# Kernel tuning notes

Measured on AMD Instinct MI355X. Metric: run time of the kernel, lower is better.

Reference implementation:

```python
import jax, jax.numpy as jnp
import numpy as np

T, H, I, E, K = 2048, 1024, 768, 16, 4

def setup_inputs() -> dict:
    key = jax.random.key(0)
    k1, k2, k3, k4, k5 = jax.random.split(key, 5)
    hidden_states = jax.random.normal(k1, (T, H), dtype=jnp.float32)
    top_k_index = jax.random.randint(k2, (T, K), 0, E, dtype=jnp.int64)
    top_k_weights = jax.random.uniform(k3, (T, K), dtype=jnp.float32)
    gate_up_proj = jax.random.normal(k4, (E, 2 * I, H), dtype=jnp.float32) * 0.02
    down_proj = jax.random.normal(k5, (E, H, I), dtype=jnp.float32) * 0.02
    return {"hidden_states": hidden_states, "top_k_index": top_k_index,
            "top_k_weights": top_k_weights, "gate_up_proj": gate_up_proj,
            "down_proj": down_proj}

def reference(hidden_states, top_k_index, top_k_weights, gate_up_proj, down_proj):
    # Masked dense MoE: scan over experts, each expert does full-token GEMMs
    # and a per-token combine weight (sum of routing weights where routed to e).
    # index_add over token_idx == sum over k of (mask * weight) * expert_out.
    n_experts = gate_up_proj.shape[0]

    def body(acc, xs):
        w_gu, w_d, e = xs  # [2I,H], [H,I], scalar
        gu = hidden_states @ w_gu.T                 # [T, 2I]
        gate, up = jnp.split(gu, 2, axis=-1)        # [T, I] each
        h = jax.nn.silu(gate) * up                  # [T, I]
        out = h @ w_d.T                             # [T, H]
        w_tok = jnp.sum(jnp.where(top_k_index == e, top_k_weights, 0.0), axis=-1)  # [T]
        return acc + out * w_tok[:, None], None

    acc0 = jnp.zeros_like(hidden_states)
    final, _ = jax.lax.scan(body, acc0, (gate_up_proj, down_proj, jnp.arange(n_experts)))
    return final
```

## Files before the change

kernel.cpp:

```cpp
#include <hip/hip_runtime.h>
#include <hip/hip_bf16.h>
#include <stdint.h>

#define T_TOK 2048
#define H_DIM 1024
#define I_DIM 768
#define E_NUM 16
#define K_TOP 4
#define NSLOT (T_TOK * K_TOP)
#define PSLOT 10240
#define NTILE 80

typedef short  s16x8 __attribute__((ext_vector_type(8)));
typedef float  f32x4 __attribute__((ext_vector_type(4)));
typedef unsigned short u16x8 __attribute__((ext_vector_type(8)));

#define MEMFENCE asm volatile("" ::: "memory")

__device__ __forceinline__ void gload16(const void* g, void* l) {
  __builtin_amdgcn_global_load_lds(
      (const __attribute__((address_space(1))) uint32_t*)g,
      (__attribute__((address_space(3))) uint32_t*)l, 16, 0, 0);
}

__device__ __forceinline__ unsigned short f2bf(float f) {
  __hip_bfloat16 h = __float2bfloat16(f);
  return *reinterpret_cast<unsigned short*>(&h);
}

__device__ __forceinline__ void write_b_row(char* bregion, int r, int half,
                                            f32x4 f0, f32x4 f1, f32x4 f2, f32x4 f3) {
  u16x8 c0, c1;
  c0[0]=f2bf(f0[0]); c0[1]=f2bf(f0[1]); c0[2]=f2bf(f0[2]); c0[3]=f2bf(f0[3]);
  c0[4]=f2bf(f1[0]); c0[5]=f2bf(f1[1]); c0[6]=f2bf(f1[2]); c0[7]=f2bf(f1[3]);
  c1[0]=f2bf(f2[0]); c1[1]=f2bf(f2[1]); c1[2]=f2bf(f2[2]); c1[3]=f2bf(f2[3]);
  c1[4]=f2bf(f3[0]); c1[5]=f2bf(f3[1]); c1[6]=f2bf(f3[2]); c1[7]=f2bf(f3[3]);
  int xr = (r >> 1) & 3;
  char* wb = bregion + r * 64;
  *(u16x8*)(wb + (((2*half + 0) ^ xr) * 16)) = c0;
  *(u16x8*)(wb + (((2*half + 1) ^ xr) * 16)) = c1;
}

__global__ __launch_bounds__(256) void cvt_bf16_kernel(
    const float* __restrict__ in, unsigned short* __restrict__ out, int n8) {
  int i = blockIdx.x * 256 + threadIdx.x;
  if (i >= n8) return;
  const float4* p = (const float4*)in;
  float4 a = p[2 * (size_t)i];
  float4 b = p[2 * (size_t)i + 1];
  u16x8 o;
  o[0] = f2bf(a.x); o[1] = f2bf(a.y); o[2] = f2bf(a.z); o[3] = f2bf(a.w);
  o[4] = f2bf(b.x); o[5] = f2bf(b.y); o[6] = f2bf(b.z); o[7] = f2bf(b.w);
  *(u16x8*)(out + (size_t)i * 8) = o;
}

__global__ __launch_bounds__(256) void route_kernel(
    const int* __restrict__ idx, const float* __restrict__ wts,
    int* __restrict__ slot_tok, float* __restrict__ slot_w,
    int* __restrict__ slot_of, int* __restrict__ tile_expert) {
  __shared__ int cnt[256][16];
  __shared__ int tot[16];
  __shared__ int pb[17];
  int tid = threadIdx.x;

  for (int e = 0; e < 16; ++e) cnt[tid][e] = 0;
  const int s0 = tid * 32;
  for (int i = 0; i < 32; ++i) {
    int e = idx[s0 + i] & 15;
    cnt[tid][e]++;
  }
  __syncthreads();
  if (tid < 16) {
    int run = 0;
    for (int c = 0; c < 256; ++c) { int v = cnt[c][tid]; cnt[c][tid] = run; run += v; }
    tot[tid] = run;
  }
  __syncthreads();
  if (tid == 0) {
    int acc = 0;
    for (int e = 0; e < 16; ++e) { pb[e] = acc; acc += (tot[e] + 127) & ~127; }
    pb[16] = acc;
  }
  __syncthreads();
  for (int p = tid; p < PSLOT; p += 256) { slot_tok[p] = 0; slot_w[p] = 0.0f; }
  if (tid < NTILE) {
    int ef = -1;
    for (int e = 0; e < 16; ++e)
      if (tid * 128 >= pb[e] && tid * 128 < pb[e + 1]) ef = e;
    tile_expert[tid] = ef;
  }
  __syncthreads();
  for (int i = 0; i < 32; ++i) {
    int s = s0 + i;
    int e = idx[s] & 15;
    int pos = pb[e] + cnt[tid][e]++;
    slot_tok[pos] = s >> 2;
    slot_w[pos]   = wts[s];
    slot_of[s]    = pos;
  }
}


__global__ __launch_bounds__(256) void gemm1_kernel(
    const unsigned short* __restrict__ Xbf,
    const float* __restrict__ Wgu,
    const int* __restrict__ slot_tok,
    const int* __restrict__ tile_expert,
    unsigned short* __restrict__ hbuf) {
  int bid  = blockIdx.y * 12 + blockIdx.x;
  int sbid = (bid & 7) * 120 + (bid >> 3);
  int by   = sbid / 12;
  int bx   = sbid % 12;
  int e = tile_expert[by];
  if (e < 0) return;
  int m0 = by * 128;
  int tid = threadIdx.x;
  int lane = tid & 63, w = tid >> 6;
  int wr = w >> 1, wc = w & 1;

  __shared__ short lds[2 * 8192];
  char* buf0 = (char*)lds;
  char* buf1 = buf0 + 16384;

  int srow = tid >> 2;
  int swzc = ((tid & 3) ^ ((tid >> 3) & 3)) * 16;
  int tok0 = slot_tok[m0 + srow];
  int tok1 = slot_tok[m0 + 64 + srow];
  const char* gA0 = (const char*)(Xbf + (size_t)tok0 * H_DIM) + swzc;
  const char* gA1 = (const char*)(Xbf + (size_t)tok1 * H_DIM) + swzc;

  int brow = tid >> 1;
  int half = tid & 1;
  int prow = (brow < 64) ? (bx * 64 + brow) : (768 + bx * 64 + (brow - 64));
  const float* gB = Wgu + ((size_t)e * 1536 + prow) * H_DIM + half * 16;

  int pswz = ((lane >> 4) ^ (((lane & 15) >> 1) & 3)) * 8;

  f32x4 accg[4][2] = {};
  f32x4 accu[4][2] = {};
  f32x4 s0_0, s0_1, s0_2, s0_3, s1_0, s1_1, s1_2, s1_3;
  f32x4 s2_0, s2_1, s2_2, s2_3, s3_0, s3_1, s3_2, s3_3;

#define NT1 32
#define A_GLOAD1(kt, bufp) do {                               \
    int kk_ = (kt) < NT1 ? (kt) : NT1 - 1;                    \
    int ko_ = kk_ * 64;                                       \
    gload16(gA0 + ko_, (bufp) + tid * 16);                    \
    gload16(gA1 + ko_, (bufp) + 4096 + tid * 16);             \
  } while (0)
#define B_LOAD1(v0, v1, v2, v3, kt) do {                      \
    int kk_ = (kt) < NT1 ? (kt) : NT1 - 1;                    \
    const f32x4* p_ = (const f32x4*)(gB + (size_t)kk_ * 32);  \
    v0 = p_[0]; v1 = p_[1]; v2 = p_[2]; v3 = p_[3];           \
  } while (0)

#define G1_COMPUTE(bufp) do {                                                          \
    const short* La = (const short*)(bufp);                                            \
    s16x8 af[4], bgf[2], buf2[2];                                                      \
    _Pragma("unroll")                                                                  \
    for (int mi = 0; mi < 4; ++mi)                                                     \
      af[mi] = *(const s16x8*)(La + (wr * 64 + mi * 16 + (lane & 15)) * 32 + pswz);    \
    _Pragma("unroll")                                                                  \
    for (int ni = 0; ni < 2; ++ni) {                                                   \
      int row = wc * 32 + ni * 16 + (lane & 15);                                       \
      bgf[ni]  = *(const s16x8*)(La + 4096 + row * 32 + pswz);                         \
      buf2[ni] = *(const s16x8*)(La + 6144 + row * 32 + pswz);                         \
    }                                                                                  \
    _Pragma("unroll")                                                                  \
    for (int mi = 0; mi < 4; ++mi)                                                     \
      _Pragma("unroll")                                                                \
      for (int ni = 0; ni < 2; ++ni) {                                                 \
        accg[mi][ni] = __builtin_amdgcn_mfma_f32_16x16x32_bf16(af[mi], bgf[ni],  accg[mi][ni], 0, 0, 0); \
        accu[mi][ni] = __builtin_amdgcn_mfma_f32_16x16x32_bf16(af[mi], buf2[ni], accu[mi][ni], 0, 0, 0); \
      }                                                                                \
  } while (0)

#define ITER1(kt, wv0, wv1, wv2, wv3, lv0, lv1, lv2, lv3) do {  \
    char* cbuf_ = ((kt) & 1) ? buf1 : buf0;                     \
    char* nbuf_ = ((kt) & 1) ? buf0 : buf1;                     \
    MEMFENCE;                                                   \
    A_GLOAD1((kt) + 1, nbuf_);                                  \
    MEMFENCE;                                                   \
    B_LOAD1(lv0, lv1, lv2, lv3, (kt) + 3);                      \
    asm volatile("s_waitcnt vmcnt(10)" ::: "memory");           \
    write_b_row(nbuf_ + 8192, brow, half, wv0, wv1, wv2, wv3);  \
    asm volatile("s_waitcnt lgkmcnt(0)" ::: "memory");          \
    __builtin_amdgcn_s_barrier();                               \
    MEMFENCE;                                                   \
    G1_COMPUTE(cbuf_);                                          \
    MEMFENCE;                                                   \
    __builtin_amdgcn_s_barrier();                               \
  } while (0)

  A_GLOAD1(0, buf0);
  MEMFENCE;
  B_LOAD1(s0_0, s0_1, s0_2, s0_3, 0);
  MEMFENCE;
  B_LOAD1(s1_0, s1_1, s1_2, s1_3, 1);
  MEMFENCE;
  B_LOAD1(s2_0, s2_1, s2_2, s2_3, 2);
  asm volatile("s_waitcnt vmcnt(8)" ::: "memory");
  write_b_row(buf0 + 8192, brow, half, s0_0, s0_1, s0_2, s0_3);

  for (int kt = 0; kt < NT1; kt += 4) {
    ITER1(kt + 0, s1_0, s1_1, s1_2, s1_3, s3_0, s3_1, s3_2, s3_3);
    ITER1(kt + 1, s2_0, s2_1, s2_2, s2_3, s0_0, s0_1, s0_2, s0_3);
    ITER1(kt + 2, s3_0, s3_1, s3_2, s3_3, s1_0, s1_1, s1_2, s1_3);
    ITER1(kt + 3, s0_0, s0_1, s0_2, s0_3, s2_0, s2_1, s2_2, s2_3);
  }
#undef ITER1
#undef G1_COMPUTE
#undef B_LOAD1
#undef A_GLOAD1

#pragma unroll
  for (int mi = 0; mi < 4; ++mi) {
#pragma unroll
    for (int ni = 0; ni < 2; ++ni) {
      int col = bx * 64 + wc * 32 + ni * 16 + (lane & 15);
#pragma unroll
      for (int q = 0; q < 4; ++q) {
        int m = m0 + wr * 64 + mi * 16 + (lane >> 4) * 4 + q;
        float g = accg[mi][ni][q];
        float u = accu[mi][ni][q];
        float s = g / (1.0f + __expf(-g));
        hbuf[(size_t)m * I_DIM + col] = f2bf(s * u);
      }
    }
  }
}

__global__ __launch_bounds__(256) void gemm2_kernel(
    const unsigned short* __restrict__ hbuf,
    const float* __restrict__ Wd,
    const int* __restrict__ slot_tok,
    const float* __restrict__ slot_w,
    const int* __restrict__ tile_expert,
    float* __restrict__ y) {
  int bid  = blockIdx.y * 8 + blockIdx.x;
  int sbid = (bid & 7) * 80 + (bid >> 3);
  int by   = sbid >> 3;
  int bx   = sbid & 7;
  int e = tile_expert[by];
  if (e < 0) return;
  int m0 = by * 128;
  int tid = threadIdx.x;
  int lane = tid & 63, w = tid >> 6;
  int wr = w >> 1, wc = w & 1;

  __shared__ short lds[2 * 8192];
  char* buf0 = (char*)lds;
  char* buf1 = buf0 + 16384;

  int srow = tid >> 2;
  int swzc = ((tid & 3) ^ ((tid >> 3) & 3)) * 16;
  const char* gA0 = (const char*)(hbuf + (size_t)(m0 + srow) * I_DIM) + swzc;
  const char* gA1 = (const char*)(hbuf + (size_t)(m0 + 64 + srow) * I_DIM) + swzc;

  int brow = tid >> 1;
  int half = tid & 1;
  const float* gB = Wd + ((size_t)e * 1024 + bx * 128 + brow) * I_DIM + half * 16;

  int pswz = ((lane >> 4) ^ (((lane & 15) >> 1) & 3)) * 8;

  f32x4 acc[4][4] = {};
  f32x4 s0_0, s0_1, s0_2, s0_3, s1_0, s1_1, s1_2, s1_3;
  f32x4 s2_0, s2_1, s2_2, s2_3, s3_0, s3_1, s3_2, s3_3;

#define NT2 24
#define A_GLOAD2(kt, bufp) do {                               \
    int kk_ = (kt) < NT2 ? (kt) : NT2 - 1;                    \
    int ko_ = kk_ * 64;                                       \
    gload16(gA0 + ko_, (bufp) + tid * 16);                    \
    gload16(gA1 + ko_, (bufp) + 4096 + tid * 16);             \
  } while (0)
#define B_LOAD2(v0, v1, v2, v3, kt) do {                      \
    int kk_ = (kt) < NT2 ? (kt) : NT2 - 1;                    \
    const f32x4* p_ = (const f32x4*)(gB + (size_t)kk_ * 32);  \
    v0 = p_[0]; v1 = p_[1]; v2 = p_[2]; v3 = p_[3];           \
  } while (0)

#define G2_COMPUTE(bufp) do {                                                          \
    const short* La = (const short*)(bufp);                                            \
    s16x8 af[4], bf[4];                                                                \
    _Pragma("unroll")                                                                  \
    for (int mi = 0; mi < 4; ++mi)                                                     \
      af[mi] = *(const s16x8*)(La + (wr * 64 + mi * 16 + (lane & 15)) * 32 + pswz);    \
    _Pragma("unroll")                                                                  \
    for (int ni = 0; ni < 4; ++ni)                                                     \
      bf[ni] = *(const s16x8*)(La + 4096 + (wc * 64 + ni * 16 + (lane & 15)) * 32 + pswz); \
    _Pragma("unroll")                                                                  \
    for (int mi = 0; mi < 4; ++mi)                                                     \
      _Pragma("unroll")                                                                \
      for (int ni = 0; ni < 4; ++ni)                                                   \
        acc[mi][ni] = __builtin_amdgcn_mfma_f32_16x16x32_bf16(af[mi], bf[ni], acc[mi][ni], 0, 0, 0); \
  } while (0)

#define ITER2(kt, wv0, wv1, wv2, wv3, lv0, lv1, lv2, lv3) do {  \
    char* cbuf_ = ((kt) & 1) ? buf1 : buf0;                     \
    char* nbuf_ = ((kt) & 1) ? buf0 : buf1;                     \
    MEMFENCE;                                                   \
    A_GLOAD2((kt) + 1, nbuf_);                                  \
    MEMFENCE;                                                   \
    B_LOAD2(lv0, lv1, lv2, lv3, (kt) + 3);                      \
    asm volatile("s_waitcnt vmcnt(10)" ::: "memory");           \
    write_b_row(nbuf_ + 8192, brow, half, wv0, wv1, wv2, wv3);  \
    asm volatile("s_waitcnt lgkmcnt(0)" ::: "memory");          \
    __builtin_amdgcn_s_barrier();                               \
    MEMFENCE;                                                   \
    G2_COMPUTE(cbuf_);                                          \
    MEMFENCE;                                                   \
    __builtin_amdgcn_s_barrier();                               \
  } while (0)

  A_GLOAD2(0, buf0);
  MEMFENCE;
  B_LOAD2(s0_0, s0_1, s0_2, s0_3, 0);
  MEMFENCE;
  B_LOAD2(s1_0, s1_1, s1_2, s1_3, 1);
  MEMFENCE;
  B_LOAD2(s2_0, s2_1, s2_2, s2_3, 2);
  asm volatile("s_waitcnt vmcnt(8)" ::: "memory");
  write_b_row(buf0 + 8192, brow, half, s0_0, s0_1, s0_2, s0_3);

  for (int kt = 0; kt < NT2; kt += 4) {
    ITER2(kt + 0, s1_0, s1_1, s1_2, s1_3, s3_0, s3_1, s3_2, s3_3);
    ITER2(kt + 1, s2_0, s2_1, s2_2, s2_3, s0_0, s0_1, s0_2, s0_3);
    ITER2(kt + 2, s3_0, s3_1, s3_2, s3_3, s1_0, s1_1, s1_2, s1_3);
    ITER2(kt + 3, s0_0, s0_1, s0_2, s0_3, s2_0, s2_1, s2_2, s2_3);
  }
#undef ITER2
#undef G2_COMPUTE
#undef B_LOAD2
#undef A_GLOAD2

#pragma unroll
  for (int mi = 0; mi < 4; ++mi) {
#pragma unroll
    for (int q = 0; q < 4; ++q) {
      int m = m0 + wr * 64 + mi * 16 + (lane >> 4) * 4 + q;
      float wgt = slot_w[m];
      float* orow = y + (size_t)m * H_DIM + bx * 128 + wc * 64 + (lane & 15);
#pragma unroll
      for (int ni = 0; ni < 4; ++ni)
        orow[ni * 16] = acc[mi][ni][q] * wgt;
    }
  }
}

__global__ __launch_bounds__(256) void combine_kernel(
    const float* __restrict__ y, const int* __restrict__ slot_of,
    float* __restrict__ out) {
  int t = blockIdx.x;
  int c = threadIdx.x * 4;
  int s0 = slot_of[t * 4 + 0], s1 = slot_of[t * 4 + 1];
  int s2 = slot_of[t * 4 + 2], s3 = slot_of[t * 4 + 3];
  f32x4 v0 = *(const f32x4*)(y + (size_t)s0 * H_DIM + c);
  f32x4 v1 = *(const f32x4*)(y + (size_t)s1 * H_DIM + c);
  f32x4 v2 = *(const f32x4*)(y + (size_t)s2 * H_DIM + c);
  f32x4 v3 = *(const f32x4*)(y + (size_t)s3 * H_DIM + c);
  f32x4 r = (v0 + v1) + (v2 + v3);
  *(f32x4*)(out + (size_t)t * H_DIM + c) = r;
}

extern "C" void kernel_launch(void* const* d_in, const int* in_sizes, int n_in,
                              void* d_out, int out_size, void* d_ws, size_t ws_size,
                              hipStream_t stream) {
  const float* hs       = (const float*)d_in[0];
  const int*   topk_idx = (const int*)d_in[1];
  const float* topk_w   = (const float*)d_in[2];
  const float* w_gu     = (const float*)d_in[3];
  const float* w_d      = (const float*)d_in[4];
  float* out = (float*)d_out;

  char* ws = (char*)d_ws;
  unsigned short* Xbf  = (unsigned short*)(ws);
  unsigned short* hbuf = (unsigned short*)(ws + 4194304);
  float*          y    = (float*)(ws + 19922944);
  int*   slot_tok    = (int*)(ws + 61865984);
  float* slot_w      = (float*)(ws + 61906944);
  int*   slot_of     = (int*)(ws + 61947904);
  int*   tile_expert = (int*)(ws + 61980672);

  cvt_bf16_kernel<<<1024, 256, 0, stream>>>(hs, Xbf, T_TOK * H_DIM / 8);
  route_kernel<<<1, 256, 0, stream>>>(topk_idx, topk_w, slot_tok, slot_w, slot_of, tile_expert);

  gemm1_kernel<<<dim3(12, NTILE), 256, 0, stream>>>(Xbf, w_gu, slot_tok, tile_expert, hbuf);
  gemm2_kernel<<<dim3(8, NTILE), 256, 0, stream>>>(hbuf, w_d, slot_tok, slot_w, tile_expert, y);
  combine_kernel<<<T_TOK, 256, 0, stream>>>(y, slot_of, out);
}
```

Before: 135.4 us.

## Pre-convert gate/up weights to K-tiled bf16 and enlarge gemm1 tiles

Adds a per-call kernel that converts the fp32 gate/up weights to bf16 in a K-major tiled layout, so gemm1 can stream both operands straight into LDS with direct global-to-LDS loads. gemm1 moves to 256x256 tiles with 512 threads, a 64-wide K step and double buffering in 128 KB of LDS. Routing now pads experts to 256 rows and emits a separate 128-row tile map for gemm2. The extra conversion pass reads and writes about 100 MB of weights every call, which competes with the gains from cheaper loads and fewer redundant B fetches.

After: 155.8 us. 1.15x slower.

```diff
diff --git a/kernel.cpp b/kernel.cpp
--- a/kernel.cpp
+++ b/kernel.cpp
@@ -7,13 +7,16 @@
 #define I_DIM 768
 #define E_NUM 16
 #define K_TOP 4
-#define NSLOT (T_TOK * K_TOP)
-#define PSLOT 10240
-#define NTILE 80
+#define NSLOT 8192
+#define PSLOT 12288
+#define NT256 48
+#define NT128 96
+#define RTOT_GU 24576
 
 typedef short  s16x8 __attribute__((ext_vector_type(8)));
 typedef float  f32x4 __attribute__((ext_vector_type(4)));
 typedef unsigned short u16x8 __attribute__((ext_vector_type(8)));
+typedef unsigned short u16x4 __attribute__((ext_vector_type(4)));
 
 #define MEMFENCE asm volatile("" ::: "memory")
 
@@ -26,19 +29,6 @@
 __device__ __forceinline__ unsigned short f2bf(float f) {
   __hip_bfloat16 h = __float2bfloat16(f);
   return *reinterpret_cast<unsigned short*>(&h);
-}
-
-__device__ __forceinline__ void write_b_row(char* bregion, int r, int half,
-                                            f32x4 f0, f32x4 f1, f32x4 f2, f32x4 f3) {
-  u16x8 c0, c1;
-  c0[0]=f2bf(f0[0]); c0[1]=f2bf(f0[1]); c0[2]=f2bf(f0[2]); c0[3]=f2bf(f0[3]);
-  c0[4]=f2bf(f1[0]); c0[5]=f2bf(f1[1]); c0[6]=f2bf(f1[2]); c0[7]=f2bf(f1[3]);
-  c1[0]=f2bf(f2[0]); c1[1]=f2bf(f2[1]); c1[2]=f2bf(f2[2]); c1[3]=f2bf(f2[3]);
-  c1[4]=f2bf(f3[0]); c1[5]=f2bf(f3[1]); c1[6]=f2bf(f3[2]); c1[7]=f2bf(f3[3]);
-  int xr = (r >> 1) & 3;
-  char* wb = bregion + r * 64;
-  *(u16x8*)(wb + (((2*half + 0) ^ xr) * 16)) = c0;
-  *(u16x8*)(wb + (((2*half + 1) ^ xr) * 16)) = c1;
 }
 
 __global__ __launch_bounds__(256) void cvt_bf16_kernel(
@@ -54,10 +44,34 @@
   *(u16x8*)(out + (size_t)i * 8) = o;
 }
 
+__global__ __launch_bounds__(256) void wtrans_kernel(
+    const float* __restrict__ in, unsigned short* __restrict__ out,
+    int K, int RTOT) {
+  __shared__ unsigned short tile[16 * 1024];
+  int r0 = blockIdx.x * 16;
+  int t = threadIdx.x;
+  int nf4 = 16 * K / 4;
+  const f32x4* src = (const f32x4*)(in + (size_t)r0 * K);
+  for (int i = t; i < nf4; i += 256) {
+    f32x4 v = src[i];
+    u16x4 o;
+    o[0] = f2bf(v[0]); o[1] = f2bf(v[1]); o[2] = f2bf(v[2]); o[3] = f2bf(v[3]);
+    *(u16x4*)(tile + (size_t)i * 4) = o;
+  }
+  __syncthreads();
+  int nkt = K / 64;
+  int row = t >> 4, k4 = (t & 15) * 4;
+  for (int kt = 0; kt < nkt; ++kt) {
+    u16x4 v = *(const u16x4*)(tile + row * K + kt * 64 + k4);
+    *(u16x4*)(out + ((size_t)kt * RTOT + r0 + row) * 64 + k4) = v;
+  }
+}
+
 __global__ __launch_bounds__(256) void route_kernel(
     const int* __restrict__ idx, const float* __restrict__ wts,
     int* __restrict__ slot_tok, float* __restrict__ slot_w,
-    int* __restrict__ slot_of, int* __restrict__ tile_expert) {
+    int* __restrict__ slot_of, int* __restrict__ tile_expert,
+    int* __restrict__ tile_expert128) {
   __shared__ int cnt[256][16];
   __shared__ int tot[16];
   __shared__ int pb[17];
@@ -78,16 +92,23 @@
   __syncthreads();
   if (tid == 0) {
     int acc = 0;
-    for (int e = 0; e < 16; ++e) { pb[e] = acc; acc += (tot[e] + 127) & ~127; }
+    for (int e = 0; e < 16; ++e) { pb[e] = acc; acc += (tot[e] + 255) & ~255; }
     pb[16] = acc;
   }
   __syncthreads();
   for (int p = tid; p < PSLOT; p += 256) { slot_tok[p] = 0; slot_w[p] = 0.0f; }
-  if (tid < NTILE) {
+  if (tid < NT256) {
     int ef = -1;
     for (int e = 0; e < 16; ++e)
-      if (tid * 128 >= pb[e] && tid * 128 < pb[e + 1]) ef = e;
+      if (tid * 256 >= pb[e] && tid * 256 < pb[e + 1]) ef = e;
     tile_expert[tid] = ef;
+  }
+  if (tid >= 64 && tid < 64 + NT128) {
+    int m = (tid - 64) * 128;
+    int ef = -1;
+    for (int e = 0; e < 16; ++e)
+      if (m >= pb[e] && m < pb[e + 1]) ef = e;
+    tile_expert128[tid - 64] = ef;
   }
   __syncthreads();
   for (int i = 0; i < 32; ++i) {
@@ -100,127 +121,111 @@
   }
 }
 
-
-__global__ __launch_bounds__(256) void gemm1_kernel(
+__global__ __launch_bounds__(512) void gemm1_kernel(
     const unsigned short* __restrict__ Xbf,
-    const float* __restrict__ Wgu,
+    const unsigned short* __restrict__ WguK,
     const int* __restrict__ slot_tok,
     const int* __restrict__ tile_expert,
     unsigned short* __restrict__ hbuf) {
-  int bid  = blockIdx.y * 12 + blockIdx.x;
-  int sbid = (bid & 7) * 120 + (bid >> 3);
-  int by   = sbid / 12;
-  int bx   = sbid % 12;
+  __shared__ char lds[131072];
+
+  int bid  = blockIdx.y * 6 + blockIdx.x;
+  int sbid = (bid & 7) * 36 + (bid >> 3);
+  int by = sbid / 6, bx = sbid % 6;
   int e = tile_expert[by];
   if (e < 0) return;
-  int m0 = by * 128;
-  int tid = threadIdx.x;
-  int lane = tid & 63, w = tid >> 6;
-  int wr = w >> 1, wc = w & 1;
-
-  __shared__ short lds[2 * 8192];
-  char* buf0 = (char*)lds;
-  char* buf1 = buf0 + 16384;
-
-  int srow = tid >> 2;
-  int swzc = ((tid & 3) ^ ((tid >> 3) & 3)) * 16;
-  int tok0 = slot_tok[m0 + srow];
-  int tok1 = slot_tok[m0 + 64 + srow];
-  const char* gA0 = (const char*)(Xbf + (size_t)tok0 * H_DIM) + swzc;
-  const char* gA1 = (const char*)(Xbf + (size_t)tok1 * H_DIM) + swzc;
-
-  int brow = tid >> 1;
-  int half = tid & 1;
-  int prow = (brow < 64) ? (bx * 64 + brow) : (768 + bx * 64 + (brow - 64));
-  const float* gB = Wgu + ((size_t)e * 1536 + prow) * H_DIM + half * 16;
-
-  int pswz = ((lane >> 4) ^ (((lane & 15) >> 1) & 3)) * 8;
-
-  f32x4 accg[4][2] = {};
-  f32x4 accu[4][2] = {};
-  f32x4 s0_0, s0_1, s0_2, s0_3, s1_0, s1_1, s1_2, s1_3;
-  f32x4 s2_0, s2_1, s2_2, s2_3, s3_0, s3_1, s3_2, s3_3;
-
-#define NT1 32
-#define A_GLOAD1(kt, bufp) do {                               \
-    int kk_ = (kt) < NT1 ? (kt) : NT1 - 1;                    \
-    int ko_ = kk_ * 64;                                       \
-    gload16(gA0 + ko_, (bufp) + tid * 16);                    \
-    gload16(gA1 + ko_, (bufp) + 4096 + tid * 16);             \
-  } while (0)
-#define B_LOAD1(v0, v1, v2, v3, kt) do {                      \
-    int kk_ = (kt) < NT1 ? (kt) : NT1 - 1;                    \
-    const f32x4* p_ = (const f32x4*)(gB + (size_t)kk_ * 32);  \
-    v0 = p_[0]; v1 = p_[1]; v2 = p_[2]; v3 = p_[3];           \
-  } while (0)
-
-#define G1_COMPUTE(bufp) do {                                                          \
-    const short* La = (const short*)(bufp);                                            \
-    s16x8 af[4], bgf[2], buf2[2];                                                      \
-    _Pragma("unroll")                                                                  \
-    for (int mi = 0; mi < 4; ++mi)                                                     \
-      af[mi] = *(const s16x8*)(La + (wr * 64 + mi * 16 + (lane & 15)) * 32 + pswz);    \
-    _Pragma("unroll")                                                                  \
-    for (int ni = 0; ni < 2; ++ni) {                                                   \
-      int row = wc * 32 + ni * 16 + (lane & 15);                                       \
-      bgf[ni]  = *(const s16x8*)(La + 4096 + row * 32 + pswz);                         \
-      buf2[ni] = *(const s16x8*)(La + 6144 + row * 32 + pswz);                         \
-    }                                                                                  \
-    _Pragma("unroll")                                                                  \
-    for (int mi = 0; mi < 4; ++mi)                                                     \
-      _Pragma("unroll")                                                                \
-      for (int ni = 0; ni < 2; ++ni) {                                                 \
-        accg[mi][ni] = __builtin_amdgcn_mfma_f32_16x16x32_bf16(af[mi], bgf[ni],  accg[mi][ni], 0, 0, 0); \
-        accu[mi][ni] = __builtin_amdgcn_mfma_f32_16x16x32_bf16(af[mi], buf2[ni], accu[mi][ni], 0, 0, 0); \
-      }                                                                                \
-  } while (0)
-
-#define ITER1(kt, wv0, wv1, wv2, wv3, lv0, lv1, lv2, lv3) do {  \
-    char* cbuf_ = ((kt) & 1) ? buf1 : buf0;                     \
-    char* nbuf_ = ((kt) & 1) ? buf0 : buf1;                     \
-    MEMFENCE;                                                   \
-    A_GLOAD1((kt) + 1, nbuf_);                                  \
-    MEMFENCE;                                                   \
-    B_LOAD1(lv0, lv1, lv2, lv3, (kt) + 3);                      \
-    asm volatile("s_waitcnt vmcnt(10)" ::: "memory");           \
-    write_b_row(nbuf_ + 8192, brow, half, wv0, wv1, wv2, wv3);  \
-    asm volatile("s_waitcnt lgkmcnt(0)" ::: "memory");          \
-    __builtin_amdgcn_s_barrier();                               \
-    MEMFENCE;                                                   \
-    G1_COMPUTE(cbuf_);                                          \
-    MEMFENCE;                                                   \
-    __builtin_amdgcn_s_barrier();                               \
-  } while (0)
-
-  A_GLOAD1(0, buf0);
+  int m0 = by * 256;
+  int t = threadIdx.x;
+  int lane = t & 63, w = t >> 6;
+  int wr = w >> 2, wc = w & 3;
+  int l15 = lane & 15, lhi = lane >> 4;
+
+  int rr = t >> 3;
+  int lslot16 = ((t & 7) ^ (rr & 7)) * 16;
+  const char* aS[4];
+#pragma unroll
+  for (int a = 0; a < 4; ++a) {
+    int tok = slot_tok[m0 + a * 64 + rr];
+    aS[a] = (const char*)Xbf + (size_t)tok * 2048 + lslot16;
+  }
+  const char* bS[4];
+#pragma unroll
+  for (int c = 0; c < 4; ++c) {
+    int rg = e * 1536 + ((c < 2) ? 0 : 768) + bx * 128 + (c & 1) * 64 + rr;
+    bS[c] = (const char*)WguK + (size_t)rg * 128 + lslot16;
+  }
+
+  f32x4 accg[8][2] = {};
+  f32x4 accu[8][2] = {};
+
+#define G1_STAGE(bi, kt) do {                                 \
+    char* dst = lds + (bi) * 65536 + t * 16;                  \
+    size_t ao = (size_t)(kt) * 128;                           \
+    size_t bo = (size_t)(kt) * ((size_t)RTOT_GU * 128);       \
+    MEMFENCE;                                                 \
+    gload16(aS[0] + ao, dst);                                 \
+    gload16(aS[1] + ao, dst + 8192);                          \
+    gload16(aS[2] + ao, dst + 16384);                         \
+    gload16(aS[3] + ao, dst + 24576);                         \
+    gload16(bS[0] + bo, dst + 32768);                         \
+    gload16(bS[1] + bo, dst + 40960);                         \
+    gload16(bS[2] + bo, dst + 49152);                         \
+    gload16(bS[3] + bo, dst + 57344);                         \
+    MEMFENCE;                                                 \
+  } while (0)
+
+#define G1_COMPUTE(bi) do {                                                        \
+    const short* La = (const short*)(lds + (bi) * 65536);                          \
+    const short* Lb = La + 16384;                                                  \
+    _Pragma("unroll")                                                              \
+    for (int ks = 0; ks < 2; ++ks) {                                               \
+      int p8 = (((ks) * 4 + lhi) ^ (l15 & 7)) * 8;                                 \
+      s16x8 af[8], bg[2], bu[2];                                                   \
+      _Pragma("unroll")                                                            \
+      for (int mi = 0; mi < 8; ++mi)                                               \
+        af[mi] = *(const s16x8*)(La + (wr * 128 + mi * 16 + l15) * 64 + p8);       \
+      _Pragma("unroll")                                                            \
+      for (int ni = 0; ni < 2; ++ni) {                                             \
+        bg[ni] = *(const s16x8*)(Lb + (wc * 32 + ni * 16 + l15) * 64 + p8);        \
+        bu[ni] = *(const s16x8*)(Lb + (128 + wc * 32 + ni * 16 + l15) * 64 + p8);  \
+      }                                                                            \
+      __builtin_amdgcn_s_setprio(1);                                               \
+      _Pragma("unroll")                                                            \
+      for (int mi = 0; mi < 8; ++mi)                                               \
+        _Pragma("unroll")                                                          \
+        for (int ni = 0; ni < 2; ++ni) {                                           \
+          accg[mi][ni] = __builtin_amdgcn_mfma_f32_16x16x32_bf16(af[mi], bg[ni], accg[mi][ni], 0, 0, 0); \
+          accu[mi][ni] = __builtin_amdgcn_mfma_f32_16x16x32_bf16(af[mi], bu[ni], accu[mi][ni], 0, 0, 0); \
+        }                                                                          \
+      __builtin_amdgcn_s_setprio(0);                                               \
+    }                                                                              \
+  } while (0)
+
+  G1_STAGE(0, 0);
+  asm volatile("s_waitcnt vmcnt(0)" ::: "memory");
+  __builtin_amdgcn_s_barrier();
   MEMFENCE;
-  B_LOAD1(s0_0, s0_1, s0_2, s0_3, 0);
-  MEMFENCE;
-  B_LOAD1(s1_0, s1_1, s1_2, s1_3, 1);
-  MEMFENCE;
-  B_LOAD1(s2_0, s2_1, s2_2, s2_3, 2);
-  asm volatile("s_waitcnt vmcnt(8)" ::: "memory");
-  write_b_row(buf0 + 8192, brow, half, s0_0, s0_1, s0_2, s0_3);
-
-  for (int kt = 0; kt < NT1; kt += 4) {
-    ITER1(kt + 0, s1_0, s1_1, s1_2, s1_3, s3_0, s3_1, s3_2, s3_3);
-    ITER1(kt + 1, s2_0, s2_1, s2_2, s2_3, s0_0, s0_1, s0_2, s0_3);
-    ITER1(kt + 2, s3_0, s3_1, s3_2, s3_3, s1_0, s1_1, s1_2, s1_3);
-    ITER1(kt + 3, s0_0, s0_1, s0_2, s0_3, s2_0, s2_1, s2_2, s2_3);
-  }
-#undef ITER1
+
+  int cur = 0;
+  for (int kt = 0; kt < 16; ++kt) {
+    if (kt + 1 < 16) G1_STAGE(cur ^ 1, kt + 1);
+    G1_COMPUTE(cur);
+    asm volatile("s_waitcnt vmcnt(0)" ::: "memory");
+    __builtin_amdgcn_s_barrier();
+    MEMFENCE;
+    cur ^= 1;
+  }
+#undef G1_STAGE
 #undef G1_COMPUTE
-#undef B_LOAD1
-#undef A_GLOAD1
-
-#pragma unroll
-  for (int mi = 0; mi < 4; ++mi) {
+
+#pragma unroll
+  for (int mi = 0; mi < 8; ++mi) {
 #pragma unroll
     for (int ni = 0; ni < 2; ++ni) {
-      int col = bx * 64 + wc * 32 + ni * 16 + (lane & 15);
+      int col = bx * 128 + wc * 32 + ni * 16 + l15;
 #pragma unroll
       for (int q = 0; q < 4; ++q) {
-        int m = m0 + wr * 64 + mi * 16 + (lane >> 4) * 4 + q;
+        int m = m0 + wr * 128 + mi * 16 + lhi * 4 + q;
         float g = accg[mi][ni][q];
         float u = accu[mi][ni][q];
         float s = g / (1.0f + __expf(-g));
@@ -235,13 +240,13 @@
     const float* __restrict__ Wd,
     const int* __restrict__ slot_tok,
     const float* __restrict__ slot_w,
-    const int* __restrict__ tile_expert,
+    const int* __restrict__ tile_expert128,
     float* __restrict__ y) {
   int bid  = blockIdx.y * 8 + blockIdx.x;
-  int sbid = (bid & 7) * 80 + (bid >> 3);
+  int sbid = (bid & 7) * 96 + (bid >> 3);
   int by   = sbid >> 3;
   int bx   = sbid & 7;
-  int e = tile_expert[by];
+  int e = tile_expert128[by];
   if (e < 0) return;
   int m0 = by * 128;
   int tid = threadIdx.x;
@@ -266,6 +271,18 @@
   f32x4 acc[4][4] = {};
   f32x4 s0_0, s0_1, s0_2, s0_3, s1_0, s1_1, s1_2, s1_3;
   f32x4 s2_0, s2_1, s2_2, s2_3, s3_0, s3_1, s3_2, s3_3;
+
+#define WR_BROW(bregion, r, h_, f0, f1, f2, f3) do {          \
+    u16x8 c0, c1;                                             \
+    c0[0]=f2bf(f0[0]); c0[1]=f2bf(f0[1]); c0[2]=f2bf(f0[2]); c0[3]=f2bf(f0[3]); \
+    c0[4]=f2bf(f1[0]); c0[5]=f2bf(f1[1]); c0[6]=f2bf(f1[2]); c0[7]=f2bf(f1[3]); \
+    c1[0]=f2bf(f2[0]); c1[1]=f2bf(f2[1]); c1[2]=f2bf(f2[2]); c1[3]=f2bf(f2[3]); \
+    c1[4]=f2bf(f3[0]); c1[5]=f2bf(f3[1]); c1[6]=f2bf(f3[2]); c1[7]=f2bf(f3[3]); \
+    int xr = ((r) >> 1) & 3;                                  \
+    char* wb = (bregion) + (r) * 64;                          \
+    *(u16x8*)(wb + (((2*(h_) + 0) ^ xr) * 16)) = c0;          \
+    *(u16x8*)(wb + (((2*(h_) + 1) ^ xr) * 16)) = c1;          \
+  } while (0)
 
 #define NT2 24
 #define A_GLOAD2(kt, bufp) do {                               \
@@ -304,7 +321,7 @@
     MEMFENCE;                                                   \
     B_LOAD2(lv0, lv1, lv2, lv3, (kt) + 3);                      \
     asm volatile("s_waitcnt vmcnt(10)" ::: "memory");           \
-    write_b_row(nbuf_ + 8192, brow, half, wv0, wv1, wv2, wv3);  \
+    WR_BROW(nbuf_ + 8192, brow, half, wv0, wv1, wv2, wv3);      \
     asm volatile("s_waitcnt lgkmcnt(0)" ::: "memory");          \
     __builtin_amdgcn_s_barrier();                               \
     MEMFENCE;                                                   \
@@ -321,7 +338,7 @@
   MEMFENCE;
   B_LOAD2(s2_0, s2_1, s2_2, s2_3, 2);
   asm volatile("s_waitcnt vmcnt(8)" ::: "memory");
-  write_b_row(buf0 + 8192, brow, half, s0_0, s0_1, s0_2, s0_3);
+  WR_BROW(buf0 + 8192, brow, half, s0_0, s0_1, s0_2, s0_3);
 
   for (int kt = 0; kt < NT2; kt += 4) {
     ITER2(kt + 0, s1_0, s1_1, s1_2, s1_3, s3_0, s3_1, s3_2, s3_3);
@@ -333,6 +350,7 @@
 #undef G2_COMPUTE
 #undef B_LOAD2
 #undef A_GLOAD2
+#undef WR_BROW
 
 #pragma unroll
   for (int mi = 0; mi < 4; ++mi) {
@@ -375,17 +393,21 @@
 
   char* ws = (char*)d_ws;
   unsigned short* Xbf  = (unsigned short*)(ws);
-  unsigned short* hbuf = (unsigned short*)(ws + 4194304);
-  float*          y    = (float*)(ws + 19922944);
-  int*   slot_tok    = (int*)(ws + 61865984);
-  float* slot_w      = (float*)(ws + 61906944);
-  int*   slot_of     = (int*)(ws + 61947904);
-  int*   tile_expert = (int*)(ws + 61980672);
+  unsigned short* WguK = (unsigned short*)(ws + 4194304);
+  float*          y    = (float*)(ws + 4194304);
+  unsigned short* hbuf = (unsigned short*)(ws + 54525952);
+  int*   slot_tok       = (int*)(ws + 73400320);
+  float* slot_w         = (float*)(ws + 73449472);
+  int*   slot_of        = (int*)(ws + 73498624);
+  int*   tile_expert    = (int*)(ws + 73531392);
+  int*   tile_expert128 = (int*)(ws + 73531648);
 
   cvt_bf16_kernel<<<1024, 256, 0, stream>>>(hs, Xbf, T_TOK * H_DIM / 8);
-  route_kernel<<<1, 256, 0, stream>>>(topk_idx, topk_w, slot_tok, slot_w, slot_of, tile_expert);
-
-  gemm1_kernel<<<dim3(12, NTILE), 256, 0, stream>>>(Xbf, w_gu, slot_tok, tile_expert, hbuf);
-  gemm2_kernel<<<dim3(8, NTILE), 256, 0, stream>>>(hbuf, w_d, slot_tok, slot_w, tile_expert, y);
+  route_kernel<<<1, 256, 0, stream>>>(topk_idx, topk_w, slot_tok, slot_w,
+                                      slot_of, tile_expert, tile_expert128);
+  wtrans_kernel<<<RTOT_GU / 16, 256, 0, stream>>>(w_gu, WguK, H_DIM, RTOT_GU);
+
+  gemm1_kernel<<<dim3(6, NT256), 512, 0, stream>>>(Xbf, WguK, slot_tok, tile_expert, hbuf);
+  gemm2_kernel<<<dim3(8, NT128), 256, 0, stream>>>(hbuf, w_d, slot_tok, slot_w, tile_expert128, y);
   combine_kernel<<<T_TOK, 256, 0, stream>>>(y, slot_of, out);
 }
```

## Enlarge grouped-GEMM M tile to 256 rows with 256-padded expert segments

Applied to the files above, without the earlier changes.

Routing now pads each expert's slot range to multiples of 256, and both grouped GEMMs use 256-row tiles (8 M-fragments per wave) instead of 128. Each streamed fp32 weight tile is reused across twice as many tokens, roughly halving weight reads from global memory. LDS use per block grows, and register pressure doubles the accumulators. More padding per expert wastes compute, and there are fewer blocks (48 row tiles) to fill the CUs. s_setprio is also raised around the MFMA blocks.

After: 189.3 us. 1.4x slower.

```diff
diff --git a/kernel.cpp b/kernel.cpp
--- a/kernel.cpp
+++ b/kernel.cpp
@@ -7,9 +7,9 @@
 #define I_DIM 768
 #define E_NUM 16
 #define K_TOP 4
-#define NSLOT (T_TOK * K_TOP)
-#define PSLOT 10240
-#define NTILE 80
+#define NSLOT 8192
+#define PSLOT 12288
+#define NT256 48
 
 typedef short  s16x8 __attribute__((ext_vector_type(8)));
 typedef float  f32x4 __attribute__((ext_vector_type(4)));
@@ -78,15 +78,15 @@
   __syncthreads();
   if (tid == 0) {
     int acc = 0;
-    for (int e = 0; e < 16; ++e) { pb[e] = acc; acc += (tot[e] + 127) & ~127; }
+    for (int e = 0; e < 16; ++e) { pb[e] = acc; acc += (tot[e] + 255) & ~255; }
     pb[16] = acc;
   }
   __syncthreads();
   for (int p = tid; p < PSLOT; p += 256) { slot_tok[p] = 0; slot_w[p] = 0.0f; }
-  if (tid < NTILE) {
+  if (tid < NT256) {
     int ef = -1;
     for (int e = 0; e < 16; ++e)
-      if (tid * 128 >= pb[e] && tid * 128 < pb[e + 1]) ef = e;
+      if (tid * 256 >= pb[e] && tid * 256 < pb[e + 1]) ef = e;
     tile_expert[tid] = ef;
   }
   __syncthreads();
@@ -108,45 +108,49 @@
     const int* __restrict__ tile_expert,
     unsigned short* __restrict__ hbuf) {
   int bid  = blockIdx.y * 12 + blockIdx.x;
-  int sbid = (bid & 7) * 120 + (bid >> 3);
-  int by   = sbid / 12;
-  int bx   = sbid % 12;
+  int sbid = (bid & 7) * 72 + (bid >> 3);
+  int by = sbid / 12, bx = sbid % 12;
   int e = tile_expert[by];
   if (e < 0) return;
-  int m0 = by * 128;
-  int tid = threadIdx.x;
-  int lane = tid & 63, w = tid >> 6;
+  int m0 = by * 256;
+  int t = threadIdx.x;
+  int lane = t & 63, w = t >> 6;
   int wr = w >> 1, wc = w & 1;
-
-  __shared__ short lds[2 * 8192];
-  char* buf0 = (char*)lds;
-  char* buf1 = buf0 + 16384;
-
-  int srow = tid >> 2;
-  int swzc = ((tid & 3) ^ ((tid >> 3) & 3)) * 16;
-  int tok0 = slot_tok[m0 + srow];
-  int tok1 = slot_tok[m0 + 64 + srow];
-  const char* gA0 = (const char*)(Xbf + (size_t)tok0 * H_DIM) + swzc;
-  const char* gA1 = (const char*)(Xbf + (size_t)tok1 * H_DIM) + swzc;
-
-  int brow = tid >> 1;
-  int half = tid & 1;
+  int l15 = lane & 15, lhi = lane >> 4;
+
+  __shared__ char lds[2 * 24576];
+  char* buf0 = lds;
+  char* buf1 = lds + 24576;
+
+  int arow = t >> 2;
+  int aswz = ((t & 3) ^ ((t >> 3) & 3)) * 16;
+  const char* gA[4];
+#pragma unroll
+  for (int c = 0; c < 4; ++c) {
+    int tok = slot_tok[m0 + c * 64 + arow];
+    gA[c] = (const char*)(Xbf + (size_t)tok * H_DIM) + aswz;
+  }
+
+  int brow = t >> 1;
+  int half = t & 1;
   int prow = (brow < 64) ? (bx * 64 + brow) : (768 + bx * 64 + (brow - 64));
   const float* gB = Wgu + ((size_t)e * 1536 + prow) * H_DIM + half * 16;
 
-  int pswz = ((lane >> 4) ^ (((lane & 15) >> 1) & 3)) * 8;
-
-  f32x4 accg[4][2] = {};
-  f32x4 accu[4][2] = {};
+  int pswz = (lhi ^ ((l15 >> 1) & 3)) * 8;
+
+  f32x4 accg[8][2] = {};
+  f32x4 accu[8][2] = {};
   f32x4 s0_0, s0_1, s0_2, s0_3, s1_0, s1_1, s1_2, s1_3;
   f32x4 s2_0, s2_1, s2_2, s2_3, s3_0, s3_1, s3_2, s3_3;
 
 #define NT1 32
 #define A_GLOAD1(kt, bufp) do {                               \
     int kk_ = (kt) < NT1 ? (kt) : NT1 - 1;                    \
-    int ko_ = kk_ * 64;                                       \
-    gload16(gA0 + ko_, (bufp) + tid * 16);                    \
-    gload16(gA1 + ko_, (bufp) + 4096 + tid * 16);             \
+    size_t ko_ = (size_t)kk_ * 64;                            \
+    gload16(gA[0] + ko_, (bufp) + t * 16);                    \
+    gload16(gA[1] + ko_, (bufp) + 4096 + t * 16);             \
+    gload16(gA[2] + ko_, (bufp) + 8192 + t * 16);             \
+    gload16(gA[3] + ko_, (bufp) + 12288 + t * 16);            \
   } while (0)
 #define B_LOAD1(v0, v1, v2, v3, kt) do {                      \
     int kk_ = (kt) < NT1 ? (kt) : NT1 - 1;                    \
@@ -156,23 +160,26 @@
 
 #define G1_COMPUTE(bufp) do {                                                          \
     const short* La = (const short*)(bufp);                                            \
-    s16x8 af[4], bgf[2], buf2[2];                                                      \
-    _Pragma("unroll")                                                                  \
-    for (int mi = 0; mi < 4; ++mi)                                                     \
-      af[mi] = *(const s16x8*)(La + (wr * 64 + mi * 16 + (lane & 15)) * 32 + pswz);    \
+    const short* Lb = (const short*)((bufp) + 16384);                                  \
+    s16x8 af[8], bg[2], bu[2];                                                         \
+    _Pragma("unroll")                                                                  \
+    for (int mi = 0; mi < 8; ++mi)                                                     \
+      af[mi] = *(const s16x8*)(La + (wr * 128 + mi * 16 + l15) * 32 + pswz);           \
     _Pragma("unroll")                                                                  \
     for (int ni = 0; ni < 2; ++ni) {                                                   \
-      int row = wc * 32 + ni * 16 + (lane & 15);                                       \
-      bgf[ni]  = *(const s16x8*)(La + 4096 + row * 32 + pswz);                         \
-      buf2[ni] = *(const s16x8*)(La + 6144 + row * 32 + pswz);                         \
+      int row = wc * 32 + ni * 16 + l15;                                               \
+      bg[ni] = *(const s16x8*)(Lb + row * 32 + pswz);                                  \
+      bu[ni] = *(const s16x8*)(Lb + (64 + row) * 32 + pswz);                           \
     }                                                                                  \
-    _Pragma("unroll")                                                                  \
-    for (int mi = 0; mi < 4; ++mi)                                                     \
+    __builtin_amdgcn_s_setprio(1);                                                     \
+    _Pragma("unroll")                                                                  \
+    for (int mi = 0; mi < 8; ++mi)                                                     \
       _Pragma("unroll")                                                                \
       for (int ni = 0; ni < 2; ++ni) {                                                 \
-        accg[mi][ni] = __builtin_amdgcn_mfma_f32_16x16x32_bf16(af[mi], bgf[ni],  accg[mi][ni], 0, 0, 0); \
-        accu[mi][ni] = __builtin_amdgcn_mfma_f32_16x16x32_bf16(af[mi], buf2[ni], accu[mi][ni], 0, 0, 0); \
+        accg[mi][ni] = __builtin_amdgcn_mfma_f32_16x16x32_bf16(af[mi], bg[ni], accg[mi][ni], 0, 0, 0); \
+        accu[mi][ni] = __builtin_amdgcn_mfma_f32_16x16x32_bf16(af[mi], bu[ni], accu[mi][ni], 0, 0, 0); \
       }                                                                                \
+    __builtin_amdgcn_s_setprio(0);                                                     \
   } while (0)
 
 #define ITER1(kt, wv0, wv1, wv2, wv3, lv0, lv1, lv2, lv3) do {  \
@@ -182,8 +189,8 @@
     A_GLOAD1((kt) + 1, nbuf_);                                  \
     MEMFENCE;                                                   \
     B_LOAD1(lv0, lv1, lv2, lv3, (kt) + 3);                      \
-    asm volatile("s_waitcnt vmcnt(10)" ::: "memory");           \
-    write_b_row(nbuf_ + 8192, brow, half, wv0, wv1, wv2, wv3);  \
+    asm volatile("s_waitcnt vmcnt(12)" ::: "memory");           \
+    write_b_row(nbuf_ + 16384, brow, half, wv0, wv1, wv2, wv3); \
     asm volatile("s_waitcnt lgkmcnt(0)" ::: "memory");          \
     __builtin_amdgcn_s_barrier();                               \
     MEMFENCE;                                                   \
@@ -200,7 +207,7 @@
   MEMFENCE;
   B_LOAD1(s2_0, s2_1, s2_2, s2_3, 2);
   asm volatile("s_waitcnt vmcnt(8)" ::: "memory");
-  write_b_row(buf0 + 8192, brow, half, s0_0, s0_1, s0_2, s0_3);
+  write_b_row(buf0 + 16384, brow, half, s0_0, s0_1, s0_2, s0_3);
 
   for (int kt = 0; kt < NT1; kt += 4) {
     ITER1(kt + 0, s1_0, s1_1, s1_2, s1_3, s3_0, s3_1, s3_2, s3_3);
@@ -214,13 +221,13 @@
 #undef A_GLOAD1
 
 #pragma unroll
-  for (int mi = 0; mi < 4; ++mi) {
+  for (int mi = 0; mi < 8; ++mi) {
 #pragma unroll
     for (int ni = 0; ni < 2; ++ni) {
-      int col = bx * 64 + wc * 32 + ni * 16 + (lane & 15);
+      int col = bx * 64 + wc * 32 + ni * 16 + l15;
 #pragma unroll
       for (int q = 0; q < 4; ++q) {
-        int m = m0 + wr * 64 + mi * 16 + (lane >> 4) * 4 + q;
+        int m = m0 + wr * 128 + mi * 16 + lhi * 4 + q;
         float g = accg[mi][ni][q];
         float u = accu[mi][ni][q];
         float s = g / (1.0f + __expf(-g));
@@ -233,46 +240,50 @@
 __global__ __launch_bounds__(256) void gemm2_kernel(
     const unsigned short* __restrict__ hbuf,
     const float* __restrict__ Wd,
-    const int* __restrict__ slot_tok,
     const float* __restrict__ slot_w,
     const int* __restrict__ tile_expert,
     float* __restrict__ y) {
   int bid  = blockIdx.y * 8 + blockIdx.x;
-  int sbid = (bid & 7) * 80 + (bid >> 3);
+  int sbid = (bid & 7) * 48 + (bid >> 3);
   int by   = sbid >> 3;
   int bx   = sbid & 7;
   int e = tile_expert[by];
   if (e < 0) return;
-  int m0 = by * 128;
-  int tid = threadIdx.x;
-  int lane = tid & 63, w = tid >> 6;
+  int m0 = by * 256;
+  int t = threadIdx.x;
+  int lane = t & 63, w = t >> 6;
   int wr = w >> 1, wc = w & 1;
-
-  __shared__ short lds[2 * 8192];
-  char* buf0 = (char*)lds;
-  char* buf1 = buf0 + 16384;
-
-  int srow = tid >> 2;
-  int swzc = ((tid & 3) ^ ((tid >> 3) & 3)) * 16;
-  const char* gA0 = (const char*)(hbuf + (size_t)(m0 + srow) * I_DIM) + swzc;
-  const char* gA1 = (const char*)(hbuf + (size_t)(m0 + 64 + srow) * I_DIM) + swzc;
-
-  int brow = tid >> 1;
-  int half = tid & 1;
+  int l15 = lane & 15, lhi = lane >> 4;
+
+  __shared__ char lds[2 * 24576];
+  char* buf0 = lds;
+  char* buf1 = lds + 24576;
+
+  int arow = t >> 2;
+  int aswz = ((t & 3) ^ ((t >> 3) & 3)) * 16;
+  const char* gA[4];
+#pragma unroll
+  for (int c = 0; c < 4; ++c)
+    gA[c] = (const char*)(hbuf + (size_t)(m0 + c * 64 + arow) * I_DIM) + aswz;
+
+  int brow = t >> 1;
+  int half = t & 1;
   const float* gB = Wd + ((size_t)e * 1024 + bx * 128 + brow) * I_DIM + half * 16;
 
-  int pswz = ((lane >> 4) ^ (((lane & 15) >> 1) & 3)) * 8;
-
-  f32x4 acc[4][4] = {};
+  int pswz = (lhi ^ ((l15 >> 1) & 3)) * 8;
+
+  f32x4 acc[8][4] = {};
   f32x4 s0_0, s0_1, s0_2, s0_3, s1_0, s1_1, s1_2, s1_3;
   f32x4 s2_0, s2_1, s2_2, s2_3, s3_0, s3_1, s3_2, s3_3;
 
 #define NT2 24
 #define A_GLOAD2(kt, bufp) do {                               \
     int kk_ = (kt) < NT2 ? (kt) : NT2 - 1;                    \
-    int ko_ = kk_ * 64;                                       \
-    gload16(gA0 + ko_, (bufp) + tid * 16);                    \
-    gload16(gA1 + ko_, (bufp) + 4096 + tid * 16);             \
+    size_t ko_ = (size_t)kk_ * 64;                            \
+    gload16(gA[0] + ko_, (bufp) + t * 16);                    \
+    gload16(gA[1] + ko_, (bufp) + 4096 + t * 16);             \
+    gload16(gA[2] + ko_, (bufp) + 8192 + t * 16);             \
+    gload16(gA[3] + ko_, (bufp) + 12288 + t * 16);            \
   } while (0)
 #define B_LOAD2(v0, v1, v2, v3, kt) do {                      \
     int kk_ = (kt) < NT2 ? (kt) : NT2 - 1;                    \
@@ -282,18 +293,21 @@
 
 #define G2_COMPUTE(bufp) do {                                                          \
     const short* La = (const short*)(bufp);                                            \
-    s16x8 af[4], bf[4];                                                                \
-    _Pragma("unroll")                                                                  \
-    for (int mi = 0; mi < 4; ++mi)                                                     \
-      af[mi] = *(const s16x8*)(La + (wr * 64 + mi * 16 + (lane & 15)) * 32 + pswz);    \
+    const short* Lb = (const short*)((bufp) + 16384);                                  \
+    s16x8 af[8], bf[4];                                                                \
+    _Pragma("unroll")                                                                  \
+    for (int mi = 0; mi < 8; ++mi)                                                     \
+      af[mi] = *(const s16x8*)(La + (wr * 128 + mi * 16 + l15) * 32 + pswz);           \
     _Pragma("unroll")                                                                  \
     for (int ni = 0; ni < 4; ++ni)                                                     \
-      bf[ni] = *(const s16x8*)(La + 4096 + (wc * 64 + ni * 16 + (lane & 15)) * 32 + pswz); \
-    _Pragma("unroll")                                                                  \
-    for (int mi = 0; mi < 4; ++mi)                                                     \
+      bf[ni] = *(const s16x8*)(Lb + (wc * 64 + ni * 16 + l15) * 32 + pswz);            \
+    __builtin_amdgcn_s_setprio(1);                                                     \
+    _Pragma("unroll")                                                                  \
+    for (int mi = 0; mi < 8; ++mi)                                                     \
       _Pragma("unroll")                                                                \
       for (int ni = 0; ni < 4; ++ni)                                                   \
         acc[mi][ni] = __builtin_amdgcn_mfma_f32_16x16x32_bf16(af[mi], bf[ni], acc[mi][ni], 0, 0, 0); \
+    __builtin_amdgcn_s_setprio(0);                                                     \
   } while (0)
 
 #define ITER2(kt, wv0, wv1, wv2, wv3, lv0, lv1, lv2, lv3) do {  \
@@ -303,8 +317,8 @@
     A_GLOAD2((kt) + 1, nbuf_);                                  \
     MEMFENCE;                                                   \
     B_LOAD2(lv0, lv1, lv2, lv3, (kt) + 3);                      \
-    asm volatile("s_waitcnt vmcnt(10)" ::: "memory");           \
-    write_b_row(nbuf_ + 8192, brow, half, wv0, wv1, wv2, wv3);  \
+    asm volatile("s_waitcnt vmcnt(12)" ::: "memory");           \
+    write_b_row(nbuf_ + 16384, brow, half, wv0, wv1, wv2, wv3); \
     asm volatile("s_waitcnt lgkmcnt(0)" ::: "memory");          \
     __builtin_amdgcn_s_barrier();                               \
     MEMFENCE;                                                   \
@@ -321,7 +335,7 @@
   MEMFENCE;
   B_LOAD2(s2_0, s2_1, s2_2, s2_3, 2);
   asm volatile("s_waitcnt vmcnt(8)" ::: "memory");
-  write_b_row(buf0 + 8192, brow, half, s0_0, s0_1, s0_2, s0_3);
+  write_b_row(buf0 + 16384, brow, half, s0_0, s0_1, s0_2, s0_3);
 
   for (int kt = 0; kt < NT2; kt += 4) {
     ITER2(kt + 0, s1_0, s1_1, s1_2, s1_3, s3_0, s3_1, s3_2, s3_3);
@@ -335,12 +349,12 @@
 #undef A_GLOAD2
 
 #pragma unroll
-  for (int mi = 0; mi < 4; ++mi) {
+  for (int mi = 0; mi < 8; ++mi) {
 #pragma unroll
     for (int q = 0; q < 4; ++q) {
-      int m = m0 + wr * 64 + mi * 16 + (lane >> 4) * 4 + q;
+      int m = m0 + wr * 128 + mi * 16 + lhi * 4 + q;
       float wgt = slot_w[m];
-      float* orow = y + (size_t)m * H_DIM + bx * 128 + wc * 64 + (lane & 15);
+      float* orow = y + (size_t)m * H_DIM + bx * 128 + wc * 64 + l15;
 #pragma unroll
       for (int ni = 0; ni < 4; ++ni)
         orow[ni * 16] = acc[mi][ni][q] * wgt;
@@ -376,16 +390,17 @@
   char* ws = (char*)d_ws;
   unsigned short* Xbf  = (unsigned short*)(ws);
   unsigned short* hbuf = (unsigned short*)(ws + 4194304);
-  float*          y    = (float*)(ws + 19922944);
-  int*   slot_tok    = (int*)(ws + 61865984);
-  float* slot_w      = (float*)(ws + 61906944);
-  int*   slot_of     = (int*)(ws + 61947904);
-  int*   tile_expert = (int*)(ws + 61980672);
+  float*          y    = (float*)(ws + 23068672);
+  int*   slot_tok    = (int*)(ws + 73400320);
+  float* slot_w      = (float*)(ws + 73449472);
+  int*   slot_of     = (int*)(ws + 73498624);
+  int*   tile_expert = (int*)(ws + 73531392);
 
   cvt_bf16_kernel<<<1024, 256, 0, stream>>>(hs, Xbf, T_TOK * H_DIM / 8);
-  route_kernel<<<1, 256, 0, stream>>>(topk_idx, topk_w, slot_tok, slot_w, slot_of, tile_expert);
-
-  gemm1_kernel<<<dim3(12, NTILE), 256, 0, stream>>>(Xbf, w_gu, slot_tok, tile_expert, hbuf);
-  gemm2_kernel<<<dim3(8, NTILE), 256, 0, stream>>>(hbuf, w_d, slot_tok, slot_w, tile_expert, y);
+  route_kernel<<<1, 256, 0, stream>>>(topk_idx, topk_w, slot_tok, slot_w,
+                                      slot_of, tile_expert);
+
+  gemm1_kernel<<<dim3(12, NT256), 256, 0, stream>>>(Xbf, w_gu, slot_tok, tile_expert, hbuf);
+  gemm2_kernel<<<dim3(8, NT256), 256, 0, stream>>>(hbuf, w_d, slot_w, tile_expert, y);
   combine_kernel<<<T_TOK, 256, 0, stream>>>(y, slot_of, out);
 }
```
